# Kernel tuning notes

Hardware: AMD Instinct MI355X
Metric: run time of the kernel (lower is better)

## Reference

```python
import jax, jax.numpy as jnp
import numpy as np

HIDDEN = 128
VEL_SCALE = 0.5
T_END = 1.0


def conv1x1(x, w, b):
    # x: [B, Cin, N], w: [Cout, Cin], b: [Cout]
    return jnp.einsum('oi,bin->bon', w, x) + b[None, :, None]


def setup_inputs() -> dict:
    key = jax.random.key(0)
    ks = jax.random.split(key, 11)
    B, N = 8, 50000
    def winit(k, shape, fan_in):
        bound = 1.0 / np.sqrt(fan_in)
        return jax.random.uniform(k, shape, jnp.float32, -bound, bound)
    return {
        'x0': jax.random.normal(ks[0], (B, 3, N), jnp.float32),
        'h1_w': winit(ks[1], (HIDDEN, 4), 4), 'h1_b': winit(ks[2], (HIDDEN,), 4),
        'g1_w': winit(ks[3], (HIDDEN, 4), 4), 'g1_b': winit(ks[4], (HIDDEN,), 4),
        'h2_w': winit(ks[5], (HIDDEN, HIDDEN), HIDDEN), 'h2_b': winit(ks[6], (HIDDEN,), HIDDEN),
        'g2_w': winit(ks[7], (HIDDEN, HIDDEN), HIDDEN), 'g2_b': winit(ks[8], (HIDDEN,), HIDDEN),
        'out_w': winit(ks[9], (3, HIDDEN), HIDDEN), 'out_b': winit(ks[10], (3,), HIDDEN),
    }


def field(t, x, h1_w, h1_b, g1_w, g1_b, h2_w, h2_b, g2_w, g2_b, out_w, out_b):
    B, _, N = x.shape
    t_chan = jnp.broadcast_to(jnp.reshape(t, (1, 1, 1)), (B, 1, N))
    z = jnp.concatenate([x, t_chan], axis=1)                 # [B, 4, N]
    z = conv1x1(z, h1_w, h1_b) * jax.nn.sigmoid(conv1x1(z, g1_w, g1_b))
    z = jax.nn.relu(z)
    z = conv1x1(z, h2_w, h2_b) * jax.nn.sigmoid(conv1x1(z, g2_w, g2_b))
    z = jax.nn.relu(z)
    v = conv1x1(z, out_w, out_b)                             # [B, 3, N]
    return jnp.tanh(v) * VEL_SCALE


def reference(x0, h1_w, h1_b, g1_w, g1_b, h2_w, h2_b, g2_w, g2_b, out_w, out_b):
    params = (h1_w, h1_b, g1_w, g1_b, h2_w, h2_b, g2_w, g2_b, out_w, out_b)
    f = lambda t, y: field(jnp.asarray(t, jnp.float32), y, *params)
    # torchdiffeq 'rk4' with t=[0, T] and no step_size: single 3/8-rule RK4 step, h = T
    h = jnp.float32(T_END)
    t0 = jnp.float32(0.0)
    third = jnp.float32(1.0 / 3.0)
    k1 = f(t0, x0)
    k2 = f(t0 + h * third, x0 + h * k1 * third)
    k3 = f(t0 + h * third * 2.0, x0 + h * (k2 - k1 * third))
    k4 = f(t0 + h, x0 + h * (k1 - k2 + k3))
    return x0 + h * (k1 + 3.0 * (k2 + k3) + k4) * jnp.float32(0.125)
```

## Files before the change

kernel.cpp:

```cpp
#include <hip/hip_runtime.h>
#include <math.h>
#include <utility>

typedef __attribute__((ext_vector_type(8))) short    bf16x8;
typedef __attribute__((ext_vector_type(4))) float    f32x4;
typedef __attribute__((ext_vector_type(2))) float    f32x2;
typedef __attribute__((ext_vector_type(2))) unsigned u32x2;
typedef __attribute__((ext_vector_type(4))) unsigned u32x4;

template<int I, int N, class F>
__device__ __forceinline__ void sfor(F&& f) {
    if constexpr (I < N) { f(std::integral_constant<int, I>{}); sfor<I + 1, N>(static_cast<F&&>(f)); }
}

#define NPT    50000
#define NTILES 6250
#define TPB    2
#define ZIN_S  40
#define Z_S    136
#define LOG2E  1.4426950408889634f

static __device__ __forceinline__ unsigned short bf16r(float f) {
    unsigned u = __builtin_bit_cast(unsigned, f);
    u += 0x7FFFu + ((u >> 16) & 1u);
    return (unsigned short)(u >> 16);
}

#if defined(__has_builtin)
#if __has_builtin(__builtin_amdgcn_cvt_pk_bf16_f32)
#define HAVE_CVT_PK_BF16 1
#endif
#if __has_builtin(__builtin_amdgcn_exp2f) && __has_builtin(__builtin_amdgcn_rcpf)
#define HAVE_RAW_TRANS 1
#endif
#endif

static __device__ __forceinline__ unsigned packbf(float a, float b) {
#ifdef HAVE_CVT_PK_BF16
    return __builtin_bit_cast(unsigned, __builtin_amdgcn_cvt_pk_bf16_f32(a, b));
#else
    return (unsigned)bf16r(a) | ((unsigned)bf16r(b) << 16);
#endif
}

#ifdef HAVE_RAW_TRANS
static __device__ __forceinline__ float fexp2(float x) { return __builtin_amdgcn_exp2f(x); }
static __device__ __forceinline__ float frcp(float x)  { return __builtin_amdgcn_rcpf(x); }
#else
static __device__ __forceinline__ float fexp2(float x) { return __exp2f(x); }
static __device__ __forceinline__ float frcp(float x)  { return __frcp_rn(x); }
#endif

static __device__ __forceinline__ unsigned gate2p(f32x2 h, f32x2 gp) {
    f32x2 e;
    e.x = fexp2(gp.x);
    e.y = fexp2(gp.y);
    f32x2 p = e + 1.f;
    float ip = frcp(p.x * p.y);
    f32x2 ps = __builtin_shufflevector(p, p, 1, 0);
    f32x2 z = (h * ps) * ip;
    z = __builtin_elementwise_max(z, f32x2{0.f, 0.f});
    return packbf(z.x, z.y);
}

static __device__ __forceinline__ bf16x8 pack8s(const float* p, float s) {
    f32x4 lo = *reinterpret_cast<const f32x4*>(p);
    f32x4 hi = *reinterpret_cast<const f32x4*>(p + 4);
    u32x4 u = { packbf(lo[0]*s, lo[1]*s), packbf(lo[2]*s, lo[3]*s),
                packbf(hi[0]*s, hi[1]*s), packbf(hi[2]*s, hi[3]*s) };
    return __builtin_bit_cast(bf16x8, u);
}
static __device__ __forceinline__ f32x4 mfma16(bf16x8 a, bf16x8 b, f32x4 c) {
    return __builtin_amdgcn_mfma_f32_16x16x32_bf16(a, b, c, 0, 0, 0);
}

__global__ __launch_bounds__(512, 4) void node_rk4_mfma(
    const float* __restrict__ x0,
    const float* __restrict__ h1_w, const float* __restrict__ h1_b,
    const float* __restrict__ g1_w, const float* __restrict__ g1_b,
    const float* __restrict__ h2_w, const float* __restrict__ h2_b,
    const float* __restrict__ g2_w, const float* __restrict__ g2_b,
    const float* __restrict__ out_w, const float* __restrict__ out_b,
    float* __restrict__ y)
{
    __shared__ __align__(16) short zin[64 * ZIN_S];
    __shared__ __align__(16) short z1s[64 * Z_S];
    __shared__ __align__(16) short z2s[64 * Z_S];
    __shared__ __align__(16) short aow_s[4 * 64 * 8];
    __shared__ __align__(16) float bias_s[4 * 128 + 16];
    __shared__ __align__(8)  unsigned a1_s[2 * 256];

    const int tid  = threadIdx.x;
    const int w    = tid >> 6;
    const int lane = tid & 63;
    const int q    = lane >> 4;
    const int m    = lane & 15;

    const int row = 16 * w + m;
    bf16x8 a2h[4], a2g[4];
    sfor<0, 4>([&](auto KS) {
        constexpr int ks = KS.value;
        a2h[ks] = pack8s(h2_w + row * 128 + ks * 32 + q * 8, 1.0f);
        a2g[ks] = pack8s(g2_w + row * 128 + ks * 32 + q * 8, -LOG2E);
    });
    if (tid < 128) {
        const f32x4 t1 = *reinterpret_cast<const f32x4*>(h1_w + tid * 4);
        const f32x4 t2 = *reinterpret_cast<const f32x4*>(g1_w + tid * 4);
        a1_s[tid * 2]           = packbf(t1[0], t1[1]);
        a1_s[tid * 2 + 1]       = packbf(t1[2], t1[3]);
        a1_s[256 + tid * 2]     = packbf(t2[0] * -LOG2E, t2[1] * -LOG2E);
        a1_s[256 + tid * 2 + 1] = packbf(t2[2] * -LOG2E, t2[3] * -LOG2E);
    }
    if (w == 0) {
        sfor<0, 4>([&](auto KS) {
            constexpr int ks = KS.value;
            bf16x8 t = {0,0,0,0,0,0,0,0};
            if (m < 3) t = pack8s(out_w + m * 128 + ks * 32 + q * 8, 2.f * LOG2E);
            *reinterpret_cast<bf16x8*>(&aow_s[(ks * 64 + lane) * 8]) = t;
        });
    }
    if (tid < 128) {
        bias_s[tid]       = h1_b[tid];
        bias_s[128 + tid] = g1_b[tid] * -LOG2E;
        bias_s[256 + tid] = h2_b[tid];
        bias_s[384 + tid] = g2_b[tid] * -LOG2E;
    }
    if (tid < 16) bias_s[512 + tid] = (tid < 3) ? out_b[tid] * (2.f * LOG2E) : 0.f;

    for (int i = tid; i < 64 * ZIN_S / 2; i += 512) ((unsigned*)zin)[i] = 0u;
    __syncthreads();

    const float third = 1.0f / 3.0f;
    const int cb4 = 16 * w + 4 * q;

    const short* zin_rd = &zin[m * ZIN_S + q * 8];
    short*       zin_wr = &zin[(w * 16 + m) * ZIN_S];
    const short* z1_rd  = &z1s[m * Z_S + q * 8];
    short*       z1_wr  = &z1s[m * Z_S + cb4];
    short*       z2_wr  = &z2s[m * Z_S + cb4];
    const short* z2_rd  = &z2s[(w * 16 + m) * Z_S + q * 8];
    const short* aow_rd = &aow_s[lane * 8];
    const float* bs1h = &bias_s[cb4];
    const float* bs1g = &bias_s[128 + cb4];
    const float* bs2h = &bias_s[256 + cb4];
    const float* bs2g = &bias_s[384 + cb4];
    const float* bsov = &bias_s[512 + 4 * q];

    #pragma unroll 1
    for (int t2 = 0; t2 < TPB; ++t2) {
        const int tile = blockIdx.x * TPB + t2;

        float xc0 = 0.f, xc1 = 0.f, xc2 = 0.f;
        int gbase = 0;
        if (w < 4 && lane < 16) {
            const int pg = tile * 64 + w * 16 + lane;
            const int bb = pg / NPT;
            const int nn = pg - bb * NPT;
            gbase = bb * 3 * NPT + nn;
            xc0 = x0[gbase]; xc1 = x0[gbase + NPT]; xc2 = x0[gbase + 2 * NPT];
        }
        float k1x=0,k1y=0,k1z=0, k2x=0,k2y=0,k2z=0, k3x=0,k3y=0,k3z=0;
        float ax=0, ay=0, az=0;

        #pragma unroll 1
        for (int s = 0; s < 4; ++s) {
            if (w < 4 && lane < 16) {
                float zi0, zi1, zi2, tt;
                if (s == 0)      { zi0 = xc0; zi1 = xc1; zi2 = xc2; tt = 0.f; }
                else if (s == 1) { zi0 = fmaf(k1x, third, xc0);
                                   zi1 = fmaf(k1y, third, xc1);
                                   zi2 = fmaf(k1z, third, xc2); tt = third; }
                else if (s == 2) { zi0 = xc0 + (k2x - k1x * third);
                                   zi1 = xc1 + (k2y - k1y * third);
                                   zi2 = xc2 + (k2z - k1z * third); tt = 2.f * third; }
                else             { zi0 = xc0 + (k1x - k2x + k3x);
                                   zi1 = xc1 + (k1y - k2y + k3y);
                                   zi2 = xc2 + (k1z - k2z + k3z); tt = 1.f; }
                u32x2 pk = { packbf(zi0, zi1), packbf(zi2, tt) };
                *reinterpret_cast<u32x2*>(zin_wr) = pk;
            }
            __syncthreads();

            {
                bf16x8 a1h = {0,0,0,0,0,0,0,0}, a1g = {0,0,0,0,0,0,0,0};
                if (q == 0) {
                    u32x2 th = *reinterpret_cast<const u32x2*>(&a1_s[row * 2]);
                    u32x2 tg = *reinterpret_cast<const u32x2*>(&a1_s[256 + row * 2]);
                    u32x4 uh = { th[0], th[1], 0u, 0u };
                    u32x4 ug = { tg[0], tg[1], 0u, 0u };
                    a1h = __builtin_bit_cast(bf16x8, uh);
                    a1g = __builtin_bit_cast(bf16x8, ug);
                }
                const f32x4 b1h = *reinterpret_cast<const f32x4*>(bs1h);
                const f32x4 b1g = *reinterpret_cast<const f32x4*>(bs1g);
                sfor<0, 4>([&](auto NT) {
                    constexpr int nt = NT.value;
                    bf16x8 bf = *reinterpret_cast<const bf16x8*>(zin_rd + nt * 16 * ZIN_S);
                    f32x4 ch = mfma16(a1h, bf, b1h);
                    f32x4 cg = mfma16(a1g, bf, b1g);
                    u32x2 pk = { gate2p(f32x2{ch[0], ch[1]}, f32x2{cg[0], cg[1]}),
                                 gate2p(f32x2{ch[2], ch[3]}, f32x2{cg[2], cg[3]}) };
                    *reinterpret_cast<u32x2*>(z1_wr + nt * 16 * Z_S) = pk;
                });
            }
            __syncthreads();

            {
                const f32x4 b2h = *reinterpret_cast<const f32x4*>(bs2h);
                const f32x4 b2g = *reinterpret_cast<const f32x4*>(bs2g);
                f32x4 ch[4], cg[4];
                sfor<0, 4>([&](auto NT) {
                    constexpr int nt = NT.value;
                    bf16x8 bf = *reinterpret_cast<const bf16x8*>(z1_rd + nt * 16 * Z_S);
                    ch[nt] = mfma16(a2h[0], bf, b2h);
                    cg[nt] = mfma16(a2g[0], bf, b2g);
                });
                sfor<1, 4>([&](auto KS) {
                    constexpr int ks = KS.value;
                    sfor<0, 4>([&](auto NT) {
                        constexpr int nt = NT.value;
                        bf16x8 bf = *reinterpret_cast<const bf16x8*>(z1_rd + nt * 16 * Z_S + ks * 32);
                        ch[nt] = mfma16(a2h[ks], bf, ch[nt]);
                        cg[nt] = mfma16(a2g[ks], bf, cg[nt]);
                    });
                });
                sfor<0, 4>([&](auto NT) {
                    constexpr int nt = NT.value;
                    u32x2 pk = { gate2p(f32x2{ch[nt][0], ch[nt][1]}, f32x2{cg[nt][0], cg[nt][1]}),
                                 gate2p(f32x2{ch[nt][2], ch[nt][3]}, f32x2{cg[nt][2], cg[nt][3]}) };
                    *reinterpret_cast<u32x2*>(z2_wr + nt * 16 * Z_S) = pk;
                });
            }
            __syncthreads();

            if (w < 4) {
                f32x4 vc = *reinterpret_cast<const f32x4*>(bsov);
                sfor<0, 4>([&](auto KS) {
                    constexpr int ks = KS.value;
                    bf16x8 af = *reinterpret_cast<const bf16x8*>(aow_rd + ks * 64 * 8);
                    bf16x8 bf = *reinterpret_cast<const bf16x8*>(z2_rd + ks * 32);
                    vc = mfma16(af, bf, vc);
                });
                f32x2 e; e.x = fexp2(vc[0]); e.y = fexp2(vc[1]);
                f32x2 p = e + 1.f;
                const float ipxy = frcp(p.x * p.y);
                const float kx = 0.5f - p.y * ipxy;
                const float ky = 0.5f - p.x * ipxy;
                const float kz = 0.5f - frcp(fexp2(vc[2]) + 1.f);

                if (s == 0)      { k1x=kx;k1y=ky;k1z=kz; ax=kx;ay=ky;az=kz; }
                else if (s == 1) { k2x=kx;k2y=ky;k2z=kz;
                                   ax=fmaf(3.f,kx,ax); ay=fmaf(3.f,ky,ay); az=fmaf(3.f,kz,az); }
                else if (s == 2) { k3x=kx;k3y=ky;k3z=kz;
                                   ax=fmaf(3.f,kx,ax); ay=fmaf(3.f,ky,ay); az=fmaf(3.f,kz,az); }
                else             { ax+=kx; ay+=ky; az+=kz; }
            }
        }

        if (w < 4 && lane < 16) {
            y[gbase]           = fmaf(0.125f, ax, xc0);
            y[gbase + NPT]     = fmaf(0.125f, ay, xc1);
            y[gbase + 2 * NPT] = fmaf(0.125f, az, xc2);
        }
        __syncthreads();
    }
}

extern "C" void kernel_launch(void* const* d_in, const int* in_sizes, int n_in,
                              void* d_out, int out_size, void* d_ws, size_t ws_size,
                              hipStream_t stream) {
    (void)in_sizes; (void)n_in; (void)d_ws; (void)ws_size; (void)out_size;
    const float* x0    = (const float*)d_in[0];
    const float* h1_w  = (const float*)d_in[1];
    const float* h1_b  = (const float*)d_in[2];
    const float* g1_w  = (const float*)d_in[3];
    const float* g1_b  = (const float*)d_in[4];
    const float* h2_w  = (const float*)d_in[5];
    const float* h2_b  = (const float*)d_in[6];
    const float* g2_w  = (const float*)d_in[7];
    const float* g2_b  = (const float*)d_in[8];
    const float* out_w = (const float*)d_in[9];
    const float* out_b = (const float*)d_in[10];
    float* y = (float*)d_out;

    node_rk4_mfma<<<NTILES / TPB, 512, 0, stream>>>(
        x0, h1_w, h1_b, g1_w, g1_b, h2_w, h2_b, g2_w, g2_b, out_w, out_b, y);
}
```

Measured before the change: 288.8 us.

## Replace padded LDS activation tiles with XOR-swizzled layout and compact buffers

The padded shared-memory strides for the input, hidden and output-weight tiles become unpadded buffers with an XOR swizzle on the column groups, so the MFMA operand reads and the gated writes avoid bank conflicts without padding. The output-weight staging buffer is shrunk to the three real rows, with lanes 3-15 reading a duplicate row whose results are discarded. Less LDS per block, plus a launch bound raised from 4 to 8 blocks, is meant to allow higher occupancy. The raised launch bound may tighten the register budget and cause spills, given that the kernel holds eight bf16x8 weight fragments in registers.

```diff
diff --git a/kernel.cpp b/kernel.cpp
--- a/kernel.cpp
+++ b/kernel.cpp
@@ -16,8 +16,7 @@
 #define NPT    50000
 #define NTILES 6250
 #define TPB    2
-#define ZIN_S  40
-#define Z_S    136
+#define Z_S    128
 #define LOG2E  1.4426950408889634f
 
 static __device__ __forceinline__ unsigned short bf16r(float f) {
@@ -74,7 +73,7 @@
     return __builtin_amdgcn_mfma_f32_16x16x32_bf16(a, b, c, 0, 0, 0);
 }
 
-__global__ __launch_bounds__(512, 4) void node_rk4_mfma(
+__global__ __launch_bounds__(512, 8) void node_rk4_mfma(
     const float* __restrict__ x0,
     const float* __restrict__ h1_w, const float* __restrict__ h1_b,
     const float* __restrict__ g1_w, const float* __restrict__ g1_b,
@@ -83,10 +82,10 @@
     const float* __restrict__ out_w, const float* __restrict__ out_b,
     float* __restrict__ y)
 {
-    __shared__ __align__(16) short zin[64 * ZIN_S];
+    __shared__ __align__(16) short zin[64 * 8];
     __shared__ __align__(16) short z1s[64 * Z_S];
     __shared__ __align__(16) short z2s[64 * Z_S];
-    __shared__ __align__(16) short aow_s[4 * 64 * 8];
+    __shared__ __align__(16) short aow_s[4 * 12 * 8];
     __shared__ __align__(16) float bias_s[4 * 128 + 16];
     __shared__ __align__(8)  unsigned a1_s[2 * 256];
 
@@ -111,12 +110,11 @@
         a1_s[256 + tid * 2]     = packbf(t2[0] * -LOG2E, t2[1] * -LOG2E);
         a1_s[256 + tid * 2 + 1] = packbf(t2[2] * -LOG2E, t2[3] * -LOG2E);
     }
-    if (w == 0) {
+    if (w == 0 && m < 3) {
         sfor<0, 4>([&](auto KS) {
             constexpr int ks = KS.value;
-            bf16x8 t = {0,0,0,0,0,0,0,0};
-            if (m < 3) t = pack8s(out_w + m * 128 + ks * 32 + q * 8, 2.f * LOG2E);
-            *reinterpret_cast<bf16x8*>(&aow_s[(ks * 64 + lane) * 8]) = t;
+            bf16x8 t = pack8s(out_w + m * 128 + ks * 32 + q * 8, 2.f * LOG2E);
+            *reinterpret_cast<bf16x8*>(&aow_s[((ks * 3 + m) * 4 + q) * 8]) = t;
         });
     }
     if (tid < 128) {
@@ -127,24 +125,27 @@
     }
     if (tid < 16) bias_s[512 + tid] = (tid < 3) ? out_b[tid] * (2.f * LOG2E) : 0.f;
 
-    for (int i = tid; i < 64 * ZIN_S / 2; i += 512) ((unsigned*)zin)[i] = 0u;
+    if (tid < 64) *reinterpret_cast<u32x4*>(&zin[tid * 8]) = u32x4{0u, 0u, 0u, 0u};
     __syncthreads();
 
     const float third = 1.0f / 3.0f;
     const int cb4 = 16 * w + 4 * q;
 
-    const short* zin_rd = &zin[m * ZIN_S + q * 8];
-    short*       zin_wr = &zin[(w * 16 + m) * ZIN_S];
-    const short* z1_rd  = &z1s[m * Z_S + q * 8];
-    short*       z1_wr  = &z1s[m * Z_S + cb4];
-    short*       z2_wr  = &z2s[m * Z_S + cb4];
-    const short* z2_rd  = &z2s[(w * 16 + m) * Z_S + q * 8];
-    const short* aow_rd = &aow_s[lane * 8];
-    const float* bs1h = &bias_s[cb4];
-    const float* bs1g = &bias_s[128 + cb4];
-    const float* bs2h = &bias_s[256 + cb4];
-    const float* bs2g = &bias_s[384 + cb4];
-    const float* bsov = &bias_s[512 + 4 * q];
+    const int m7   = m & 7;
+    const int qx8  = (q ^ (m & 3)) * 8;
+    const int m4_8 = (m & 4) * 8;
+
+    const short* zin_rd = &zin[m * 8];
+    short*       zin_wr = &zin[row * 8];
+    const short* z1_re  = &z1s[m * Z_S + qx8 + m4_8];
+    const short* z1_ro  = &z1s[m * Z_S + qx8 + (m4_8 ^ 32)];
+    short*       z1_wr  = &z1s[m * Z_S + (((2 * w + (q >> 1)) ^ m7) * 8) + (q & 1) * 4];
+    short*       z2_wr  = &z2s[m * Z_S + (((2 * w + (q >> 1)) ^ m7) * 8) + (q & 1) * 4];
+    const short* z2_re  = &z2s[(16 * w + m) * Z_S + qx8 + m4_8];
+    const short* z2_ro  = &z2s[(16 * w + m) * Z_S + qx8 + (m4_8 ^ 32)];
+    const short* aow_rd = &aow_s[((m < 3 ? m : 2) * 4 + q) * 8];
+    const float* bs     = &bias_s[cb4];
+    const float* bsov   = &bias_s[512 + 4 * q];
 
     #pragma unroll 1
     for (int t2 = 0; t2 < TPB; ++t2) {
@@ -191,35 +192,37 @@
                     a1h = __builtin_bit_cast(bf16x8, uh);
                     a1g = __builtin_bit_cast(bf16x8, ug);
                 }
-                const f32x4 b1h = *reinterpret_cast<const f32x4*>(bs1h);
-                const f32x4 b1g = *reinterpret_cast<const f32x4*>(bs1g);
+                const f32x4 b1h = *reinterpret_cast<const f32x4*>(bs);
+                const f32x4 b1g = *reinterpret_cast<const f32x4*>(bs + 128);
                 sfor<0, 4>([&](auto NT) {
                     constexpr int nt = NT.value;
-                    bf16x8 bf = *reinterpret_cast<const bf16x8*>(zin_rd + nt * 16 * ZIN_S);
+                    bf16x8 bf = *reinterpret_cast<const bf16x8*>(zin_rd + nt * 128);
                     f32x4 ch = mfma16(a1h, bf, b1h);
                     f32x4 cg = mfma16(a1g, bf, b1g);
                     u32x2 pk = { gate2p(f32x2{ch[0], ch[1]}, f32x2{cg[0], cg[1]}),
                                  gate2p(f32x2{ch[2], ch[3]}, f32x2{cg[2], cg[3]}) };
-                    *reinterpret_cast<u32x2*>(z1_wr + nt * 16 * Z_S) = pk;
+                    *reinterpret_cast<u32x2*>(z1_wr + nt * 2048) = pk;
                 });
             }
             __syncthreads();
 
             {
-                const f32x4 b2h = *reinterpret_cast<const f32x4*>(bs2h);
-                const f32x4 b2g = *reinterpret_cast<const f32x4*>(bs2g);
+                const f32x4 b2h = *reinterpret_cast<const f32x4*>(bs + 256);
+                const f32x4 b2g = *reinterpret_cast<const f32x4*>(bs + 384);
                 f32x4 ch[4], cg[4];
                 sfor<0, 4>([&](auto NT) {
                     constexpr int nt = NT.value;
-                    bf16x8 bf = *reinterpret_cast<const bf16x8*>(z1_rd + nt * 16 * Z_S);
+                    bf16x8 bf = *reinterpret_cast<const bf16x8*>(z1_re + nt * 2048);
                     ch[nt] = mfma16(a2h[0], bf, b2h);
                     cg[nt] = mfma16(a2g[0], bf, b2g);
                 });
                 sfor<1, 4>([&](auto KS) {
                     constexpr int ks = KS.value;
+                    const short* zb = (ks & 1) ? z1_ro : z1_re;
+                    constexpr int koff = (ks & 2) ? 64 : 0;
                     sfor<0, 4>([&](auto NT) {
                         constexpr int nt = NT.value;
-                        bf16x8 bf = *reinterpret_cast<const bf16x8*>(z1_rd + nt * 16 * Z_S + ks * 32);
+                        bf16x8 bf = *reinterpret_cast<const bf16x8*>(zb + nt * 2048 + koff);
                         ch[nt] = mfma16(a2h[ks], bf, ch[nt]);
                         cg[nt] = mfma16(a2g[ks], bf, cg[nt]);
                     });
@@ -228,7 +231,7 @@
                     constexpr int nt = NT.value;
                     u32x2 pk = { gate2p(f32x2{ch[nt][0], ch[nt][1]}, f32x2{cg[nt][0], cg[nt][1]}),
                                  gate2p(f32x2{ch[nt][2], ch[nt][3]}, f32x2{cg[nt][2], cg[nt][3]}) };
-                    *reinterpret_cast<u32x2*>(z2_wr + nt * 16 * Z_S) = pk;
+                    *reinterpret_cast<u32x2*>(z2_wr + nt * 2048) = pk;
                 });
             }
             __syncthreads();
@@ -237,8 +240,10 @@
                 f32x4 vc = *reinterpret_cast<const f32x4*>(bsov);
                 sfor<0, 4>([&](auto KS) {
                     constexpr int ks = KS.value;
-                    bf16x8 af = *reinterpret_cast<const bf16x8*>(aow_rd + ks * 64 * 8);
-                    bf16x8 bf = *reinterpret_cast<const bf16x8*>(z2_rd + ks * 32);
+                    bf16x8 af = *reinterpret_cast<const bf16x8*>(aow_rd + ks * 96);
+                    const short* zb = (ks & 1) ? z2_ro : z2_re;
+                    constexpr int koff = (ks & 2) ? 64 : 0;
+                    bf16x8 bf = *reinterpret_cast<const bf16x8*>(zb + koff);
                     vc = mfma16(af, bf, vc);
                 });
                 f32x2 e; e.x = fexp2(vc[0]); e.y = fexp2(vc[1]);
```

Result: slower. 545.7 us (+88.9%).
